# Kernel optimization log

Measured on AMD Instinct MI355X. Metric: run time of the kernel, lower is better.

Reference implementation:

```python
import jax, jax.numpy as jnp
import numpy as np

B, S, D, H, F, E = 8, 1024, 1024, 16, 3584, 2
HD = D // H
NUM_LABELS = 2
EPS = 1e-6


def setup_inputs() -> dict:
    key = jax.random.key(0)
    ks = jax.random.split(key, 10)
    w = lambda k, shape: jax.random.normal(k, shape, jnp.float32) * 0.02
    return {
        "hidden_states": jax.random.normal(ks[0], (B, S, D), jnp.float32),
        "ln1_w": jnp.ones((D,), jnp.float32),
        "q_w": w(ks[1], (D, D)),
        "k_w": w(ks[2], (D, D)),
        "v_w": w(ks[3], (D, D)),
        "o_w": w(ks[4], (D, D)),
        "ln2_w": jnp.ones((D,), jnp.float32),
        "router_w": w(ks[5], (D, E)),
        "gate_w": w(ks[6], (E, D, F)),
        "up_w": w(ks[7], (E, D, F)),
        "down_w": w(ks[8], (E, F, D)),
        "final_ln_w": jnp.ones((D,), jnp.float32),
        "score_w": w(ks[9], (D, NUM_LABELS)),
    }


def rmsnorm(x, w):
    var = jnp.mean(jnp.square(x), axis=-1, keepdims=True)
    return x * jax.lax.rsqrt(var + EPS) * w


def reference(hidden_states, ln1_w, q_w, k_w, v_w, o_w, ln2_w, router_w,
              gate_w, up_w, down_w, final_ln_w, score_w):
    x = hidden_states  # [B,S,D]
    # --- attention block (Jamba attention: no RoPE, no bias, causal) ---
    res = x
    h = rmsnorm(x, ln1_w)
    q = (h @ q_w).reshape(B, S, H, HD).transpose(0, 2, 1, 3)  # [B,H,S,HD]
    k = (h @ k_w).reshape(B, S, H, HD).transpose(0, 2, 1, 3)
    v = (h @ v_w).reshape(B, S, H, HD).transpose(0, 2, 1, 3)
    scores = jnp.einsum("bhqd,bhkd->bhqk", q, k) / np.sqrt(HD).astype(np.float32)
    causal = jnp.tril(jnp.ones((S, S), bool))
    scores = jnp.where(causal, scores, jnp.finfo(jnp.float32).min)
    attn = jax.nn.softmax(scores, axis=-1)
    ctx = jnp.einsum("bhqk,bhkd->bhqd", attn, v)
    attn_out = ctx.transpose(0, 2, 1, 3).reshape(B, S, D) @ o_w
    x = res + attn_out
    # --- top-1 MoE FFN (Jamba: softmax router, top-k, NO renormalization) ---
    res = x
    h = rmsnorm(x, ln2_w).reshape(B * S, D)
    router_logits = h @ router_w  # [N,E]
    probs = jax.nn.softmax(router_logits.astype(jnp.float32), axis=-1)
    top_w = jnp.max(probs, axis=-1)       # top-1 weight
    sel = jnp.argmax(probs, axis=-1)      # selected expert id
    moe = jnp.zeros_like(h)
    for e in range(E):  # fixed tiny loop over experts
        y = (jax.nn.silu(h @ gate_w[e]) * (h @ up_w[e])) @ down_w[e]
        moe = moe + jnp.where(sel == e, top_w, 0.0)[:, None] * y
    x = res + moe.reshape(B, S, D)
    # --- final RMSNorm + score head on first token ---
    x = rmsnorm(x, final_ln_w)
    logits = x[:, 0, :] @ score_w  # [B, NUM_LABELS]
    return logits
```

## Files before the change

### kernel.cpp

```cpp
#include <hip/hip_runtime.h>
#include <math.h>

#define B 8
#define S 1024
#define D 1024
#define F 3584

#define KSV 64
#define CHV 16
#define KS5 32
#define CH5 32
#define KS6 224
#define CH6 16

typedef float f4v __attribute__((ext_vector_type(4)));
#define LD4(p) (*(const f4v*)(p))

#define FMA4(A, s, W) { (A).x += (s)*(W).x; (A).y += (s)*(W).y; (A).z += (s)*(W).z; (A).w += (s)*(W).w; }

#define BB8(bb, ACC, XS, CH, koff) { \
  f4v xa = LD4((XS) + (bb)*(CH) + (koff)); \
  f4v xb = LD4((XS) + (bb)*(CH) + (koff) + 4); \
  FMA4(ACC, xa.x, w0); FMA4(ACC, xa.y, w1); FMA4(ACC, xa.z, w2); FMA4(ACC, xa.w, w3); \
  FMA4(ACC, xb.x, w4); FMA4(ACC, xb.y, w5); FMA4(ACC, xb.z, w6); FMA4(ACC, xb.w, w7); }

#define ALL8(XS, CH, koff) \
  BB8(0, acc0, XS, CH, koff) BB8(1, acc1, XS, CH, koff) \
  BB8(2, acc2, XS, CH, koff) BB8(3, acc3, XS, CH, koff) \
  BB8(4, acc4, XS, CH, koff) BB8(5, acc5, XS, CH, koff) \
  BB8(6, acc6, XS, CH, koff) BB8(7, acc7, XS, CH, koff)

__device__ __forceinline__ float block_sum256(float v, volatile float* buf) {
  #pragma unroll
  for (int o = 32; o; o >>= 1) v += __shfl_down(v, o);
  __syncthreads();
  if ((threadIdx.x & 63) == 0) buf[threadIdx.x >> 6] = v;
  __syncthreads();
  return buf[0] + buf[1] + buf[2] + buf[3];
}

template<int NT>
__device__ __forceinline__ f4v wld(const f4v* p) {
  if constexpr (NT) return __builtin_nontemporal_load(p);
  else return *p;
}

__device__ __forceinline__ void prefetch_llc(const float* __restrict__ w,
                                             int nf4, int pid, int nblk,
                                             int tid, float* __restrict__ dummy) {
  const f4v* p = (const f4v*)w;
  int stride = nblk * 256;
  f4v acc = {0.f, 0.f, 0.f, 0.f};
  for (int i = pid * 256 + tid; i < nf4; i += stride) acc += p[i];
  float t = acc.x + acc.y + acc.z + acc.w;
  if (t > 1e30f) dummy[0] = t;
}

template<int NT>
__device__ __forceinline__ void mv16(const float* __restrict__ W, int j,
                                     float* __restrict__ Pout,
                                     const float* xs,
                                     const int* ssel, int e) {
  const f4v* Wp = (const f4v*)(W + j);
  const int st = D / 4;
  f4v acc0 = {0,0,0,0}, acc1 = {0,0,0,0}, acc2 = {0,0,0,0}, acc3 = {0,0,0,0};
  f4v acc4 = {0,0,0,0}, acc5 = {0,0,0,0}, acc6 = {0,0,0,0}, acc7 = {0,0,0,0};
  f4v w0 = wld<NT>(Wp+0*st), w1 = wld<NT>(Wp+1*st), w2 = wld<NT>(Wp+2*st), w3 = wld<NT>(Wp+3*st);
  f4v w4 = wld<NT>(Wp+4*st), w5 = wld<NT>(Wp+5*st), w6 = wld<NT>(Wp+6*st), w7 = wld<NT>(Wp+7*st);
  f4v v0 = wld<NT>(Wp+8*st), v1 = wld<NT>(Wp+9*st), v2 = wld<NT>(Wp+10*st), v3 = wld<NT>(Wp+11*st);
  f4v v4 = wld<NT>(Wp+12*st), v5 = wld<NT>(Wp+13*st), v6 = wld<NT>(Wp+14*st), v7 = wld<NT>(Wp+15*st);
  ALL8(xs, CHV, 0);
  w0 = v0; w1 = v1; w2 = v2; w3 = v3; w4 = v4; w5 = v5; w6 = v6; w7 = v7;
  ALL8(xs, CHV, 8);
  #define MV_ST(bb, ACC) \
    if (!ssel || ssel[bb] == e) *(f4v*)(Pout + (bb)*(size_t)D + j) = ACC;
  MV_ST(0, acc0) MV_ST(1, acc1) MV_ST(2, acc2) MV_ST(3, acc3)
  MV_ST(4, acc4) MV_ST(5, acc5) MV_ST(6, acc6) MV_ST(7, acc7)
  #undef MV_ST
}

#define NF4_GATE (2 * D * F / 4)

__global__ __launch_bounds__(256, 2) void k_mvp_v(const float* __restrict__ hs,
                                                  const float* __restrict__ ln1w,
                                                  const float* __restrict__ vw,
                                                  const float* __restrict__ gw,
                                                  float* __restrict__ Vp,
                                                  float* __restrict__ dummy) {
  __shared__ float xs[8 * CHV];
  __shared__ float scsh[8];
  int tid = threadIdx.x;
  int bid = blockIdx.x;
  if (bid >= KSV) {
    prefetch_llc(gw, NF4_GATE, bid - KSV, 256 - KSV, tid, dummy);
    return;
  }
  int w = tid >> 6, lane = tid & 63;
  #pragma unroll
  for (int b2 = 0; b2 < 2; b2++) {
    int b = w * 2 + b2;
    const f4v* hp = (const f4v*)(hs + (size_t)b * S * D);
    float ss = 0.f;
    #pragma unroll
    for (int t = 0; t < 4; t++) {
      f4v v = hp[lane * 4 + t];
      ss += v.x*v.x + v.y*v.y + v.z*v.z + v.w*v.w;
    }
    #pragma unroll
    for (int o = 32; o; o >>= 1) ss += __shfl_down(ss, o);
    if (lane == 0) scsh[b] = rsqrtf(ss * (1.f / (float)D) + 1e-6f);
  }
  __syncthreads();
  int i0 = bid * CHV;
  if (tid < 128) {
    int bb = tid >> 4, ii = tid & 15;
    xs[tid] = hs[(size_t)bb * S * D + i0 + ii] * scsh[bb] * ln1w[i0 + ii];
  }
  __syncthreads();
  mv16<1>(vw + (size_t)i0 * D, tid * 4, Vp + (size_t)bid * 8 * D, xs, 0, 0);
}

__global__ __launch_bounds__(256, 2) void k_ored(const float* __restrict__ Vp,
                                                 const float* __restrict__ ow,
                                                 const float* __restrict__ uw,
                                                 float* __restrict__ Op,
                                                 float* __restrict__ dummy) {
  __shared__ float xs[8 * CHV];
  int tid = threadIdx.x;
  int bid = blockIdx.x;
  if (bid >= KSV) {
    prefetch_llc(uw, NF4_GATE, bid - KSV, 256 - KSV, tid, dummy);
    return;
  }
  int i0 = bid * CHV;
  if (tid < 128) {
    int bb = tid >> 4, ii = tid & 15;
    float s = 0.f;
    #pragma unroll 16
    for (int p = 0; p < KSV; p++) s += Vp[((size_t)p * 8 + bb) * D + i0 + ii];
    xs[bb * CHV + ii] = s;
  }
  __syncthreads();
  mv16<1>(ow + (size_t)i0 * D, tid * 4, Op + (size_t)bid * 8 * D, xs, 0, 0);
}

__global__ void k_mid(const float* __restrict__ hs, const float* __restrict__ Op,
                      const float* __restrict__ ln2, const float* __restrict__ rw,
                      const float* __restrict__ dwp,
                      float* __restrict__ xr, float* __restrict__ h2,
                      float* __restrict__ topw, int* __restrict__ sel,
                      float* __restrict__ dummy) {
  __shared__ float buf[4];
  int b = blockIdx.x;
  if (b >= 8) {
    prefetch_llc(dwp, NF4_GATE, b - 8, 248, threadIdx.x, dummy);
    return;
  }
  int idx = threadIdx.x * 4;
  f4v x = LD4(hs + (size_t)b * S * D + idx);
  #pragma unroll 16
  for (int p = 0; p < KSV; p++) {
    f4v v = LD4(Op + ((size_t)p * 8 + b) * D + idx);
    x.x += v.x; x.y += v.y; x.z += v.z; x.w += v.w;
  }
  *(f4v*)(xr + b * D + idx) = x;
  float ss = x.x*x.x + x.y*x.y + x.z*x.z + x.w*x.w;
  float tot = block_sum256(ss, buf);
  float sc = rsqrtf(tot * (1.f / (float)D) + 1e-6f);
  f4v wv = LD4(ln2 + idx);
  f4v h;
  h.x = x.x*sc*wv.x; h.y = x.y*sc*wv.y; h.z = x.z*sc*wv.z; h.w = x.w*sc*wv.w;
  *(f4v*)(h2 + b * D + idx) = h;
  float r0 = h.x * rw[idx * 2]     + h.y * rw[(idx + 1) * 2] +
             h.z * rw[(idx + 2) * 2] + h.w * rw[(idx + 3) * 2];
  float r1 = h.x * rw[idx * 2 + 1]     + h.y * rw[(idx + 1) * 2 + 1] +
             h.z * rw[(idx + 2) * 2 + 1] + h.w * rw[(idx + 3) * 2 + 1];
  r0 = block_sum256(r0, buf);
  r1 = block_sum256(r1, buf);
  if (threadIdx.x == 0) {
    float m = fmaxf(r0, r1);
    float e0 = __expf(r0 - m), e1 = __expf(r1 - m);
    float inv = 1.f / (e0 + e1);
    float p0 = e0 * inv, p1 = e1 * inv;
    topw[b] = fmaxf(p0, p1);
    sel[b] = (p1 > p0) ? 1 : 0;
  }
}

__global__ __launch_bounds__(256, 2) void k_gateup(const float* __restrict__ h2,
                                                   const float* __restrict__ gw,
                                                   const float* __restrict__ uw,
                                                   const int* __restrict__ sel,
                                                   float* __restrict__ Pgu) {
  __shared__ float xs[8 * CH5];
  __shared__ int ssel[8];
  int tid = threadIdx.x;
  int kc = blockIdx.y, colt = blockIdx.x;
  int i0 = kc * CH5;
  { int bb = tid >> 5, r = tid & 31;
    xs[tid] = h2[bb * D + i0 + r]; }
  if (tid < 8) ssel[tid] = sel[tid];
  __syncthreads();
  int c = colt * 1024 + tid * 4;
  int m = c / F;
  int j = c - m * F;
  const float* base = (m < 2 ? gw : uw) + (size_t)(m & 1) * D * F;
  const f4v* Wp = (const f4v*)(base + (size_t)i0 * F + j);
  const int st = F / 4;
  f4v acc0 = {0,0,0,0}, acc1 = {0,0,0,0}, acc2 = {0,0,0,0}, acc3 = {0,0,0,0};
  f4v acc4 = {0,0,0,0}, acc5 = {0,0,0,0}, acc6 = {0,0,0,0}, acc7 = {0,0,0,0};
  f4v w0 = Wp[0*st], w1 = Wp[1*st], w2 = Wp[2*st], w3 = Wp[3*st];
  f4v w4 = Wp[4*st], w5 = Wp[5*st], w6 = Wp[6*st], w7 = Wp[7*st];
  Wp += 8 * st;
  #pragma unroll
  for (int t = 0; t < CH5 / 8 - 1; t++) {
    f4v n0 = Wp[0*st], n1 = Wp[1*st], n2 = Wp[2*st], n3 = Wp[3*st];
    f4v n4 = Wp[4*st], n5 = Wp[5*st], n6 = Wp[6*st], n7 = Wp[7*st];
    Wp += 8 * st;
    ALL8(xs, CH5, t * 8);
    w0 = n0; w1 = n1; w2 = n2; w3 = n3; w4 = n4; w5 = n5; w6 = n6; w7 = n7;
  }
  ALL8(xs, CH5, CH5 - 8);
  int me = m & 1;
  #define GU_ST(bb, ACC) \
    if (ssel[bb] == me) \
      *(f4v*)(Pgu + (((size_t)kc * 4 + m) * 8 + (bb)) * F + j) = ACC;
  GU_ST(0, acc0) GU_ST(1, acc1) GU_ST(2, acc2) GU_ST(3, acc3)
  GU_ST(4, acc4) GU_ST(5, acc5) GU_ST(6, acc6) GU_ST(7, acc7)
  #undef GU_ST
}

__global__ __launch_bounds__(256, 2) void k_down(const float* __restrict__ Pgu,
                                                 const float* __restrict__ dw,
                                                 const int* __restrict__ sel,
                                                 float* __restrict__ Dp) {
  __shared__ float xs[8 * CH6];
  __shared__ int ssel[8];
  int tid = threadIdx.x;
  int e = blockIdx.x & 1, ch = blockIdx.x >> 1, i0 = ch * CH6;
  if (tid < 8) ssel[tid] = sel[tid];
  __syncthreads();
  if (tid < 128) {
    int bb = tid >> 4, ii = tid & 15;
    float r = 0.f;
    if (ssel[bb] == e) {
      float ga = 0.f, ua = 0.f;
      #pragma unroll
      for (int kc = 0; kc < KS5; kc++) {
        ga += Pgu[(((size_t)kc * 4 + e)     * 8 + bb) * F + i0 + ii];
        ua += Pgu[(((size_t)kc * 4 + 2 + e) * 8 + bb) * F + i0 + ii];
      }
      r = (ga / (1.f + __expf(-ga))) * ua;
    }
    xs[bb * CH6 + ii] = r;
  }
  __syncthreads();
  mv16<0>(dw + (size_t)e * F * D + (size_t)i0 * D, tid * 4,
          Dp + (((size_t)ch * 2 + e) * 8) * D, xs, ssel, e);
}

__global__ void k_final(const float* __restrict__ xr, const float* __restrict__ Dp,
                        const float* __restrict__ topw, const int* __restrict__ sel,
                        const float* __restrict__ flw, const float* __restrict__ sw,
                        float* __restrict__ out) {
  __shared__ float buf[4];
  int b = blockIdx.x;
  int e = sel[b];
  float tw = topw[b];
  int idx = threadIdx.x * 4;
  f4v y = {0,0,0,0};
  #pragma unroll 16
  for (int p = 0; p < KS6; p++) {
    f4v v = LD4(Dp + (((size_t)p * 2 + e) * 8 + b) * D + idx);
    y.x += v.x; y.y += v.y; y.z += v.z; y.w += v.w;
  }
  f4v x = LD4(xr + b * D + idx);
  x.x += tw * y.x; x.y += tw * y.y; x.z += tw * y.z; x.w += tw * y.w;
  float ss = x.x*x.x + x.y*x.y + x.z*x.z + x.w*x.w;
  float tot = block_sum256(ss, buf);
  float sc = rsqrtf(tot * (1.f / (float)D) + 1e-6f);
  f4v wv = LD4(flw + idx);
  float n0 = x.x*sc*wv.x, n1 = x.y*sc*wv.y, n2 = x.z*sc*wv.z, n3 = x.w*sc*wv.w;
  float l0 = n0 * sw[idx * 2]     + n1 * sw[(idx + 1) * 2] +
             n2 * sw[(idx + 2) * 2] + n3 * sw[(idx + 3) * 2];
  float l1 = n0 * sw[idx * 2 + 1]     + n1 * sw[(idx + 1) * 2 + 1] +
             n2 * sw[(idx + 2) * 2 + 1] + n3 * sw[(idx + 3) * 2 + 1];
  l0 = block_sum256(l0, buf);
  l1 = block_sum256(l1, buf);
  if (threadIdx.x == 0) { out[b * 2 + 0] = l0; out[b * 2 + 1] = l1; }
}

extern "C" void kernel_launch(void* const* d_in, const int* in_sizes, int n_in,
                              void* d_out, int out_size, void* d_ws, size_t ws_size,
                              hipStream_t stream) {
  const float* hs  = (const float*)d_in[0];
  const float* ln1 = (const float*)d_in[1];
  const float* vw  = (const float*)d_in[4];
  const float* ow  = (const float*)d_in[5];
  const float* ln2 = (const float*)d_in[6];
  const float* rw  = (const float*)d_in[7];
  const float* gw  = (const float*)d_in[8];
  const float* uw  = (const float*)d_in[9];
  const float* dw  = (const float*)d_in[10];
  const float* flw = (const float*)d_in[11];
  const float* sw  = (const float*)d_in[12];

  float* ws = (float*)d_ws;
  float* Vp   = ws;
  float* Op   = ws + 524288;
  float* xr   = ws + 1048576;
  float* h2   = ws + 1056768;
  float* tw8  = ws + 1064960;
  int*   sel8 = (int*)(ws + 1064968);
  float* Pgu  = ws + 1064992;
  float* Dp   = ws + 4735008;
  float* dummy = ws + 8405024;

  k_mvp_v<<<256, 256, 0, stream>>>(hs, ln1, vw, gw, Vp, dummy);
  k_ored<<<256, 256, 0, stream>>>(Vp, ow, uw, Op, dummy);
  k_mid<<<256, 256, 0, stream>>>(hs, Op, ln2, rw, dw, xr, h2, tw8, sel8, dummy);
  k_gateup<<<dim3(14, KS5), 256, 0, stream>>>(h2, gw, uw, sel8, Pgu);
  k_down<<<2 * KS6, 256, 0, stream>>>(Pgu, dw, sel8, Dp);
  k_final<<<8, 256, 0, stream>>>(xr, Dp, tw8, sel8, flw, sw, (float*)d_out);
}
```

Measured before the change: 244.7 us.

## Drop LLC prefetch blocks, use nontemporal weight loads, split final reduction

Removes the extra blocks in the first three kernels that warmed the last-level cache with the gate, up and down expert weights, so those kernels now launch only their compute blocks. The gate/up and down matvecs switch to nontemporal weight loads. The final partial-sum reduction over 224 down-projection chunks moves out of the 8-block final kernel into a new 64-block kernel that also produces per-block sums of squares. This spreads the serial reduction across more CUs but adds one more launch and loses any overlap that the cache prefetch provided.

```diff
diff --git a/kernel.cpp b/kernel.cpp
--- a/kernel.cpp
+++ b/kernel.cpp
@@ -43,17 +43,6 @@
 __device__ __forceinline__ f4v wld(const f4v* p) {
   if constexpr (NT) return __builtin_nontemporal_load(p);
   else return *p;
-}
-
-__device__ __forceinline__ void prefetch_llc(const float* __restrict__ w,
-                                             int nf4, int pid, int nblk,
-                                             int tid, float* __restrict__ dummy) {
-  const f4v* p = (const f4v*)w;
-  int stride = nblk * 256;
-  f4v acc = {0.f, 0.f, 0.f, 0.f};
-  for (int i = pid * 256 + tid; i < nf4; i += stride) acc += p[i];
-  float t = acc.x + acc.y + acc.z + acc.w;
-  if (t > 1e30f) dummy[0] = t;
 }
 
 template<int NT>
@@ -79,22 +68,14 @@
   #undef MV_ST
 }
 
-#define NF4_GATE (2 * D * F / 4)
-
 __global__ __launch_bounds__(256, 2) void k_mvp_v(const float* __restrict__ hs,
                                                   const float* __restrict__ ln1w,
                                                   const float* __restrict__ vw,
-                                                  const float* __restrict__ gw,
-                                                  float* __restrict__ Vp,
-                                                  float* __restrict__ dummy) {
+                                                  float* __restrict__ Vp) {
   __shared__ float xs[8 * CHV];
   __shared__ float scsh[8];
   int tid = threadIdx.x;
   int bid = blockIdx.x;
-  if (bid >= KSV) {
-    prefetch_llc(gw, NF4_GATE, bid - KSV, 256 - KSV, tid, dummy);
-    return;
-  }
   int w = tid >> 6, lane = tid & 63;
   #pragma unroll
   for (int b2 = 0; b2 < 2; b2++) {
@@ -122,16 +103,10 @@
 
 __global__ __launch_bounds__(256, 2) void k_ored(const float* __restrict__ Vp,
                                                  const float* __restrict__ ow,
-                                                 const float* __restrict__ uw,
-                                                 float* __restrict__ Op,
-                                                 float* __restrict__ dummy) {
+                                                 float* __restrict__ Op) {
   __shared__ float xs[8 * CHV];
   int tid = threadIdx.x;
   int bid = blockIdx.x;
-  if (bid >= KSV) {
-    prefetch_llc(uw, NF4_GATE, bid - KSV, 256 - KSV, tid, dummy);
-    return;
-  }
   int i0 = bid * CHV;
   if (tid < 128) {
     int bb = tid >> 4, ii = tid & 15;
@@ -146,16 +121,10 @@
 
 __global__ void k_mid(const float* __restrict__ hs, const float* __restrict__ Op,
                       const float* __restrict__ ln2, const float* __restrict__ rw,
-                      const float* __restrict__ dwp,
                       float* __restrict__ xr, float* __restrict__ h2,
-                      float* __restrict__ topw, int* __restrict__ sel,
-                      float* __restrict__ dummy) {
+                      float* __restrict__ topw, int* __restrict__ sel) {
   __shared__ float buf[4];
   int b = blockIdx.x;
-  if (b >= 8) {
-    prefetch_llc(dwp, NF4_GATE, b - 8, 248, threadIdx.x, dummy);
-    return;
-  }
   int idx = threadIdx.x * 4;
   f4v x = LD4(hs + (size_t)b * S * D + idx);
   #pragma unroll 16
@@ -209,13 +178,13 @@
   const int st = F / 4;
   f4v acc0 = {0,0,0,0}, acc1 = {0,0,0,0}, acc2 = {0,0,0,0}, acc3 = {0,0,0,0};
   f4v acc4 = {0,0,0,0}, acc5 = {0,0,0,0}, acc6 = {0,0,0,0}, acc7 = {0,0,0,0};
-  f4v w0 = Wp[0*st], w1 = Wp[1*st], w2 = Wp[2*st], w3 = Wp[3*st];
-  f4v w4 = Wp[4*st], w5 = Wp[5*st], w6 = Wp[6*st], w7 = Wp[7*st];
+  f4v w0 = wld<1>(Wp+0*st), w1 = wld<1>(Wp+1*st), w2 = wld<1>(Wp+2*st), w3 = wld<1>(Wp+3*st);
+  f4v w4 = wld<1>(Wp+4*st), w5 = wld<1>(Wp+5*st), w6 = wld<1>(Wp+6*st), w7 = wld<1>(Wp+7*st);
   Wp += 8 * st;
   #pragma unroll
   for (int t = 0; t < CH5 / 8 - 1; t++) {
-    f4v n0 = Wp[0*st], n1 = Wp[1*st], n2 = Wp[2*st], n3 = Wp[3*st];
-    f4v n4 = Wp[4*st], n5 = Wp[5*st], n6 = Wp[6*st], n7 = Wp[7*st];
+    f4v n0 = wld<1>(Wp+0*st), n1 = wld<1>(Wp+1*st), n2 = wld<1>(Wp+2*st), n3 = wld<1>(Wp+3*st);
+    f4v n4 = wld<1>(Wp+4*st), n5 = wld<1>(Wp+5*st), n6 = wld<1>(Wp+6*st), n7 = wld<1>(Wp+7*st);
     Wp += 8 * st;
     ALL8(xs, CH5, t * 8);
     w0 = n0; w1 = n1; w2 = n2; w3 = n3; w4 = n4; w5 = n5; w6 = n6; w7 = n7;
@@ -255,30 +224,55 @@
     xs[bb * CH6 + ii] = r;
   }
   __syncthreads();
-  mv16<0>(dw + (size_t)e * F * D + (size_t)i0 * D, tid * 4,
+  mv16<1>(dw + (size_t)e * F * D + (size_t)i0 * D, tid * 4,
           Dp + (((size_t)ch * 2 + e) * 8) * D, xs, ssel, e);
 }
 
-__global__ void k_final(const float* __restrict__ xr, const float* __restrict__ Dp,
-                        const float* __restrict__ topw, const int* __restrict__ sel,
+__global__ __launch_bounds__(256, 2) void k_dred(const float* __restrict__ xr,
+                                                 const float* __restrict__ Dp,
+                                                 const float* __restrict__ topw,
+                                                 const int* __restrict__ sel,
+                                                 float* __restrict__ x2,
+                                                 float* __restrict__ psq) {
+  __shared__ f4v sh[8][32];
+  int bb = blockIdx.x >> 3, q = blockIdx.x & 7;
+  int e = sel[bb];
+  float tw = topw[bb];
+  int t = threadIdx.x;
+  int c = t & 31, g = t >> 5;
+  int col = q * 128 + c * 4;
+  f4v acc = {0,0,0,0};
+  #pragma unroll 7
+  for (int ch = g * 28; ch < g * 28 + 28; ch++)
+    acc += LD4(Dp + (((size_t)ch * 2 + e) * 8 + bb) * D + col);
+  sh[g][c] = acc;
+  __syncthreads();
+  if (t < 32) {
+    f4v y = sh[0][t];
+    #pragma unroll
+    for (int gg = 1; gg < 8; gg++) y += sh[gg][t];
+    int colt = q * 128 + t * 4;
+    f4v x = LD4(xr + bb * D + colt);
+    x += tw * y;
+    *(f4v*)(x2 + bb * D + colt) = x;
+    float ss = x.x*x.x + x.y*x.y + x.z*x.z + x.w*x.w;
+    #pragma unroll
+    for (int o = 16; o; o >>= 1) ss += __shfl_down(ss, o, 32);
+    if (t == 0) psq[blockIdx.x] = ss;
+  }
+}
+
+__global__ void k_final(const float* __restrict__ x2, const float* __restrict__ psq,
                         const float* __restrict__ flw, const float* __restrict__ sw,
                         float* __restrict__ out) {
   __shared__ float buf[4];
   int b = blockIdx.x;
-  int e = sel[b];
-  float tw = topw[b];
+  float tot = 0.f;
+  #pragma unroll
+  for (int q = 0; q < 8; q++) tot += psq[b * 8 + q];
+  float sc = rsqrtf(tot * (1.f / (float)D) + 1e-6f);
   int idx = threadIdx.x * 4;
-  f4v y = {0,0,0,0};
-  #pragma unroll 16
-  for (int p = 0; p < KS6; p++) {
-    f4v v = LD4(Dp + (((size_t)p * 2 + e) * 8 + b) * D + idx);
-    y.x += v.x; y.y += v.y; y.z += v.z; y.w += v.w;
-  }
-  f4v x = LD4(xr + b * D + idx);
-  x.x += tw * y.x; x.y += tw * y.y; x.z += tw * y.z; x.w += tw * y.w;
-  float ss = x.x*x.x + x.y*x.y + x.z*x.z + x.w*x.w;
-  float tot = block_sum256(ss, buf);
-  float sc = rsqrtf(tot * (1.f / (float)D) + 1e-6f);
+  f4v x = LD4(x2 + b * D + idx);
   f4v wv = LD4(flw + idx);
   float n0 = x.x*sc*wv.x, n1 = x.y*sc*wv.y, n2 = x.z*sc*wv.z, n3 = x.w*sc*wv.w;
   float l0 = n0 * sw[idx * 2]     + n1 * sw[(idx + 1) * 2] +
@@ -314,12 +308,14 @@
   int*   sel8 = (int*)(ws + 1064968);
   float* Pgu  = ws + 1064992;
   float* Dp   = ws + 4735008;
-  float* dummy = ws + 8405024;
-
-  k_mvp_v<<<256, 256, 0, stream>>>(hs, ln1, vw, gw, Vp, dummy);
-  k_ored<<<256, 256, 0, stream>>>(Vp, ow, uw, Op, dummy);
-  k_mid<<<256, 256, 0, stream>>>(hs, Op, ln2, rw, dw, xr, h2, tw8, sel8, dummy);
+  float* x2   = ws + 8405024;
+  float* psq  = ws + 8413216;
+
+  k_mvp_v<<<KSV, 256, 0, stream>>>(hs, ln1, vw, Vp);
+  k_ored<<<KSV, 256, 0, stream>>>(Vp, ow, Op);
+  k_mid<<<8, 256, 0, stream>>>(hs, Op, ln2, rw, xr, h2, tw8, sel8);
   k_gateup<<<dim3(14, KS5), 256, 0, stream>>>(h2, gw, uw, sel8, Pgu);
   k_down<<<2 * KS6, 256, 0, stream>>>(Pgu, dw, sel8, Dp);
-  k_final<<<8, 256, 0, stream>>>(xr, Dp, tw8, sel8, flw, sw, (float*)d_out);
-}
+  k_dred<<<64, 256, 0, stream>>>(xr, Dp, tw8, sel8, x2, psq);
+  k_final<<<8, 256, 0, stream>>>(x2, psq, flw, sw, (float*)d_out);
+}
```

After: 211.4 us. -13.6%, faster.
